# Kernel tuning notes

Hardware: AMD Instinct MI355X
Metric: run time of the kernel (lower is better)

The kernel has to match this reference:

```python
import jax, jax.numpy as jnp
import numpy as np

# Winograd F(2x2, 3x3) transform matrices (G matches the module's self.G)
_BT = np.array([[1, 0, -1, 0], [0, 1, 1, 0], [0, -1, 1, 0], [0, 1, 0, -1]], dtype=np.float32)
_G = np.array([[1, 0, 0], [0.5, 0.5, 0.5], [0.5, -0.5, 0.5], [0, 0, 1]], dtype=np.float32)
_AT = np.array([[1, 1, 1, 0], [0, 1, -1, -1]], dtype=np.float32)

PAD = 1  # module padding


def setup_inputs() -> dict:
    key = jax.random.key(0)
    k1, k2, k3 = jax.random.split(key, 3)
    x = jax.random.normal(k1, (16, 128, 112, 112), dtype=jnp.float32)
    weight = jax.random.normal(k2, (128, 128, 3, 3), dtype=jnp.float32) * 0.05
    bias = jax.random.normal(k3, (128,), dtype=jnp.float32) * 0.05
    return {"x": x, "weight": weight, "bias": bias}


def reference(x, weight, bias):
    # Winograd F(2x2,3x3) convolution, stride=1, padding=PAD.
    N, C, H, W = x.shape
    O = weight.shape[0]
    oh = H + 2 * PAD - 2
    ow = W + 2 * PAD - 2
    nth = -(-oh // 2)  # number of 2x2 output tiles along H
    ntw = -(-ow // 2)
    Hp = 2 * nth + 2  # padded size so every tile has a full 4x4 input patch
    Wp = 2 * ntw + 2
    xp = jnp.pad(x, ((0, 0), (0, 0), (PAD, Hp - H - PAD), (PAD, Wp - W - PAD)))

    # Gather overlapping 4x4 input tiles with stride 2 -> (N, C, nth, ntw, 4, 4)
    ih = (jnp.arange(nth) * 2)[:, None] + jnp.arange(4)[None, :]
    iw = (jnp.arange(ntw) * 2)[:, None] + jnp.arange(4)[None, :]
    tiles = xp[:, :, ih[:, None, :, None], iw[None, :, None, :]]

    Bt = jnp.asarray(_BT)
    G = jnp.asarray(_G)
    At = jnp.asarray(_AT)

    # Input transform: V = B^T d B   -> (N, C, nth, ntw, 4, 4)
    V = jnp.einsum('ij,nctujk,lk->nctuil', Bt, tiles, Bt)
    # Filter transform: U = G g G^T  -> (O, C, 4, 4)
    U = jnp.einsum('ij,ocjk,lk->ocil', G, weight, G)
    # Elementwise multiply in Winograd domain, contract over input channels
    M = jnp.einsum('ocij,nctuij->notuij', U, V)
    # Output transform: y = A^T M A  -> (N, O, nth, ntw, 2, 2)
    Yt = jnp.einsum('ai,notuij,bj->notuab', At, M, At)

    # Reassemble tiles into the output image and crop to (oh, ow)
    Y = Yt.transpose(0, 1, 2, 4, 3, 5).reshape(N, O, 2 * nth, 2 * ntw)[:, :, :oh, :ow]
    return Y + bias[None, :, None, None]
```

## Files before the change

kernel.cpp:

```cpp
#include <hip/hip_runtime.h>
#include <hip/hip_bf16.h>

typedef __bf16 bf16x8 __attribute__((ext_vector_type(8)));
typedef float f32x4 __attribute__((ext_vector_type(4)));

#define HH 112
#define WW 112
#define CIN 128
#define COUT 128

#define RR 18
#define RC 18
#define CSTRIDE 40

__global__ void wino_prep_weights(const float* __restrict__ w,
                                  __hip_bfloat16* __restrict__ wb) {
    int t = blockIdx.x * 256 + threadIdx.x;
    if (t >= 9 * COUT * CIN) return;
    int c = t & (CIN - 1);
    int o = (t >> 7) & (COUT - 1);
    int r = t >> 14;
    wb[t] = __float2bfloat16(w[(o * CIN + c) * 9 + r]);
}

__global__ __launch_bounds__(256, 2) void conv3x3_mfma(
        const float* __restrict__ x, const __hip_bfloat16* __restrict__ wb,
        const float* __restrict__ bias, float* __restrict__ out) {
    __shared__ __align__(16) __hip_bfloat16 xs[RR * RC * CSTRIDE];

    const int bx = blockIdx.x, by = blockIdx.y, n = blockIdx.z;
    const int ox0 = bx * 16, oy0 = by * 16;
    const int tid = threadIdx.x;
    const int lane = tid & 63;
    const int wv = tid >> 6;
    const int wo = wv >> 1;
    const int wp = wv & 1;
    const int l15 = lane & 15;
    const int lg = lane >> 4;

    f32x4 acc[4][8];
#pragma unroll
    for (int i = 0; i < 4; ++i)
#pragma unroll
        for (int j = 0; j < 8; ++j)
            acc[i][j] = (f32x4){0.f, 0.f, 0.f, 0.f};

#pragma unroll 1
    for (int cc = 0; cc < 4; ++cc) {
        if (cc) __syncthreads();
        const int cbase = cc * 32;
#pragma unroll
        for (int it = 0; it < 3; ++it) {
            int q = tid + it * 256;
            if (q < RR * 32) {
                int c = q & 31, row = q >> 5;
                int h = oy0 - 1 + row;
                const bool hok = (unsigned)h < (unsigned)HH;
                const float* src = x + (((size_t)(n * CIN + cbase + c) * HH + h) * WW) + (ox0 - 1);
                __hip_bfloat16* dst = xs + (row * RC) * CSTRIDE + c;
#pragma unroll
                for (int col = 0; col < RC; ++col) {
                    int wc = ox0 - 1 + col;
                    float v = 0.f;
                    if (hok && (unsigned)wc < (unsigned)WW) v = src[col];
                    dst[col * CSTRIDE] = __float2bfloat16(v);
                }
            }
        }
        __syncthreads();

#pragma unroll 1
        for (int off = 0; off < 9; ++off) {
            const int dy = (off * 11) >> 5;
            const int dx = off - dy * 3;
            bf16x8 af[4];
            const __hip_bfloat16* wbase =
                wb + ((size_t)(off * COUT) + wo * 64 + l15) * CIN + cbase + lg * 8;
#pragma unroll
            for (int os = 0; os < 4; ++os)
                af[os] = *reinterpret_cast<const bf16x8*>(wbase + os * 16 * CIN);
            bf16x8 bfr[8];
#pragma unroll
            for (int ps = 0; ps < 8; ++ps) {
                int cell = (wp * 8 + ps + dy) * RC + (l15 + dx);
                bfr[ps] = *reinterpret_cast<const bf16x8*>(xs + cell * CSTRIDE + lg * 8);
            }
#pragma unroll
            for (int os = 0; os < 4; ++os)
#pragma unroll
                for (int ps = 0; ps < 8; ++ps)
                    acc[os][ps] = __builtin_amdgcn_mfma_f32_16x16x32_bf16(
                        af[os], bfr[ps], acc[os][ps], 0, 0, 0);
        }
    }

#pragma unroll
    for (int os = 0; os < 4; ++os) {
#pragma unroll
        for (int r = 0; r < 4; ++r) {
            int o = wo * 64 + os * 16 + lg * 4 + r;
            float bv = bias[o];
            float* obase = out + (((size_t)(n * COUT + o) * HH + oy0) * WW) + ox0 + l15;
#pragma unroll
            for (int ps = 0; ps < 8; ++ps) {
                int py = wp * 8 + ps;
                obase[py * WW] = acc[os][ps][r] + bv;
            }
        }
    }
}

extern "C" void kernel_launch(void* const* d_in, const int* in_sizes, int n_in,
                              void* d_out, int out_size, void* d_ws, size_t ws_size,
                              hipStream_t stream) {
    const float* x = (const float*)d_in[0];
    const float* w = (const float*)d_in[1];
    const float* bias = (const float*)d_in[2];
    float* out = (float*)d_out;
    __hip_bfloat16* wb = (__hip_bfloat16*)d_ws;

    hipLaunchKernelGGL(wino_prep_weights, dim3(576), dim3(256), 0, stream, w, wb);
    hipLaunchKernelGGL(conv3x3_mfma, dim3(7, 7, 16), dim3(256), 0, stream,
                       x, wb, bias, out);
}
```

Baseline: 366.1 us.

## Pre-transpose input to padded NHWC bf16 and double-buffer async LDS loads

Adds a pre-pass that converts the NCHW fp32 input into a zero-padded NHWC bf16 buffer in workspace. The conv kernel then fills a double-buffered LDS tile with direct global-to-LDS 16-byte loads, overlapping the next channel chunk's load with the current chunk's MFMAs. This replaces the old per-element strided fp32 loads, conversions and bounds checks. Output tiles shrink to 8 rows, which doubles the grid and raises the occupancy hint to 3, at the cost of two extra kernel launches and a full extra pass over the input.

```diff
diff --git a/kernel.cpp b/kernel.cpp
--- a/kernel.cpp
+++ b/kernel.cpp
@@ -8,10 +8,11 @@
 #define WW 112
 #define CIN 128
 #define COUT 128
+#define HP 114
+#define WP 114
 
-#define RR 18
-#define RC 18
-#define CSTRIDE 40
+#define RRV 10
+#define RCV 18
 
 __global__ void wino_prep_weights(const float* __restrict__ w,
                                   __hip_bfloat16* __restrict__ wb) {
@@ -23,13 +24,52 @@
     wb[t] = __float2bfloat16(w[(o * CIN + c) * 9 + r]);
 }
 
-__global__ __launch_bounds__(256, 2) void conv3x3_mfma(
-        const float* __restrict__ x, const __hip_bfloat16* __restrict__ wb,
+__global__ void pad_borders(__hip_bfloat16* __restrict__ xt) {
+    int q = blockIdx.x * 256 + threadIdx.x;
+    int n = blockIdx.y;
+    if (q >= 452 * 16) return;
+    int chunk = q & 15;
+    int cell = q >> 4;
+    int hp, wp;
+    if (cell < 114)      { hp = 0;          wp = cell; }
+    else if (cell < 228) { hp = 113;        wp = cell - 114; }
+    else if (cell < 340) { hp = cell - 227; wp = 0; }
+    else                 { hp = cell - 339; wp = 113; }
+    bf16x8 z = {};
+    *reinterpret_cast<bf16x8*>(xt + ((size_t)(n * HP + hp) * WP + wp) * CIN + chunk * 8) = z;
+}
+
+__global__ __launch_bounds__(256) void transpose_pad(
+        const float* __restrict__ x, __hip_bfloat16* __restrict__ xt) {
+    const int wl = threadIdx.x & 15;
+    const int cg = threadIdx.x >> 4;
+    const int w = blockIdx.x * 16 + wl;
+    const int h = blockIdx.y;
+    const int n = blockIdx.z;
+    const float* src = x + (((size_t)(n * CIN + cg * 8) * HH + h) * WW) + w;
+    float v[8];
+#pragma unroll
+    for (int j = 0; j < 8; ++j) v[j] = src[(size_t)j * HH * WW];
+    union { bf16x8 v8; __hip_bfloat16 e[8]; } o;
+#pragma unroll
+    for (int j = 0; j < 8; ++j) o.e[j] = __float2bfloat16(v[j]);
+    *reinterpret_cast<bf16x8*>(
+        xt + ((size_t)(n * HP + h + 1) * WP + (w + 1)) * CIN + cg * 8) = o.v8;
+}
+
+__device__ __forceinline__ void gload_lds16(const __hip_bfloat16* g, __hip_bfloat16* l) {
+    __builtin_amdgcn_global_load_lds(
+        (const __attribute__((address_space(1))) unsigned int*)g,
+        (__attribute__((address_space(3))) unsigned int*)l, 16, 0, 0);
+}
+
+__global__ __launch_bounds__(256, 3) void conv3x3_mfma(
+        const __hip_bfloat16* __restrict__ xt, const __hip_bfloat16* __restrict__ wb,
         const float* __restrict__ bias, float* __restrict__ out) {
-    __shared__ __align__(16) __hip_bfloat16 xs[RR * RC * CSTRIDE];
+    __shared__ __align__(16) __hip_bfloat16 xs[2][RRV * RCV * 32];
 
-    const int bx = blockIdx.x, by = blockIdx.y, n = blockIdx.z;
-    const int ox0 = bx * 16, oy0 = by * 16;
+    const int ox0 = blockIdx.x * 16, oy0 = blockIdx.y * 8;
+    const int n = blockIdx.z;
     const int tid = threadIdx.x;
     const int lane = tid & 63;
     const int wv = tid >> 6;
@@ -38,38 +78,46 @@
     const int l15 = lane & 15;
     const int lg = lane >> 4;
 
-    f32x4 acc[4][8];
+    f32x4 acc[4][4];
 #pragma unroll
     for (int i = 0; i < 4; ++i)
 #pragma unroll
-        for (int j = 0; j < 8; ++j)
-            acc[i][j] = (f32x4){0.f, 0.f, 0.f, 0.f};
+        for (int j = 0; j < 4; ++j) acc[i][j] = (f32x4){0.f, 0.f, 0.f, 0.f};
+
+    const __hip_bfloat16* gb0 = xt + (((size_t)n * HP + oy0) * WP + ox0) * CIN;
+
+    int s_row[3], s_col[3], s_sub[3], s_act[3];
+#pragma unroll
+    for (int it = 0; it < 3; ++it) {
+        int q = tid + it * 256;
+        s_act[it] = (q < RRV * RCV * 4);
+        int cell = q >> 2;
+        int row = cell / RCV;
+        s_row[it] = row;
+        s_col[it] = cell - row * RCV;
+        s_sub[it] = q & 3;
+    }
+
+    auto stage = [&](int buf, int cc) {
+        const __hip_bfloat16* gb = gb0 + cc * 32;
+#pragma unroll
+        for (int it = 0; it < 3; ++it) {
+            int q = tid + it * 256;
+            if (s_act[it])
+                gload_lds16(gb + ((size_t)(s_row[it] * WP + s_col[it])) * CIN + s_sub[it] * 8,
+                            &xs[buf][q * 8]);
+        }
+    };
+
+    stage(0, 0);
+    __syncthreads();
 
 #pragma unroll 1
     for (int cc = 0; cc < 4; ++cc) {
-        if (cc) __syncthreads();
+        if (cc < 3) stage((cc + 1) & 1, cc + 1);
+        const int buf = cc & 1;
         const int cbase = cc * 32;
 #pragma unroll
-        for (int it = 0; it < 3; ++it) {
-            int q = tid + it * 256;
-            if (q < RR * 32) {
-                int c = q & 31, row = q >> 5;
-                int h = oy0 - 1 + row;
-                const bool hok = (unsigned)h < (unsigned)HH;
-                const float* src = x + (((size_t)(n * CIN + cbase + c) * HH + h) * WW) + (ox0 - 1);
-                __hip_bfloat16* dst = xs + (row * RC) * CSTRIDE + c;
-#pragma unroll
-                for (int col = 0; col < RC; ++col) {
-                    int wc = ox0 - 1 + col;
-                    float v = 0.f;
-                    if (hok && (unsigned)wc < (unsigned)WW) v = src[col];
-                    dst[col * CSTRIDE] = __float2bfloat16(v);
-                }
-            }
-        }
-        __syncthreads();
-
-#pragma unroll 1
         for (int off = 0; off < 9; ++off) {
             const int dy = (off * 11) >> 5;
             const int dx = off - dy * 3;
@@ -79,19 +127,22 @@
 #pragma unroll
             for (int os = 0; os < 4; ++os)
                 af[os] = *reinterpret_cast<const bf16x8*>(wbase + os * 16 * CIN);
-            bf16x8 bfr[8];
+            bf16x8 bfr[4];
 #pragma unroll
-            for (int ps = 0; ps < 8; ++ps) {
-                int cell = (wp * 8 + ps + dy) * RC + (l15 + dx);
-                bfr[ps] = *reinterpret_cast<const bf16x8*>(xs + cell * CSTRIDE + lg * 8);
+            for (int ps = 0; ps < 4; ++ps) {
+                int row = wp * 4 + ps + dy;
+                int col = l15 + dx;
+                bfr[ps] = *reinterpret_cast<const bf16x8*>(
+                    &xs[buf][((row * RCV + col) * 32) + lg * 8]);
             }
 #pragma unroll
             for (int os = 0; os < 4; ++os)
 #pragma unroll
-                for (int ps = 0; ps < 8; ++ps)
+                for (int ps = 0; ps < 4; ++ps)
                     acc[os][ps] = __builtin_amdgcn_mfma_f32_16x16x32_bf16(
                         af[os], bfr[ps], acc[os][ps], 0, 0, 0);
         }
+        __syncthreads();
     }
 
 #pragma unroll
@@ -100,12 +151,10 @@
         for (int r = 0; r < 4; ++r) {
             int o = wo * 64 + os * 16 + lg * 4 + r;
             float bv = bias[o];
-            float* obase = out + (((size_t)(n * COUT + o) * HH + oy0) * WW) + ox0 + l15;
+            float* obase = out + (((size_t)(n * COUT + o) * HH + oy0 + wp * 4) * WW) + ox0 + l15;
 #pragma unroll
-            for (int ps = 0; ps < 8; ++ps) {
-                int py = wp * 8 + ps;
-                obase[py * WW] = acc[os][ps][r] + bv;
-            }
+            for (int ps = 0; ps < 4; ++ps)
+                obase[ps * WW] = acc[os][ps][r] + bv;
         }
     }
 }
@@ -117,9 +166,13 @@
     const float* w = (const float*)d_in[1];
     const float* bias = (const float*)d_in[2];
     float* out = (float*)d_out;
-    __hip_bfloat16* wb = (__hip_bfloat16*)d_ws;
+
+    __hip_bfloat16* xt = (__hip_bfloat16*)d_ws;
+    __hip_bfloat16* wb = (__hip_bfloat16*)((char*)d_ws + 53231616);
 
     hipLaunchKernelGGL(wino_prep_weights, dim3(576), dim3(256), 0, stream, w, wb);
-    hipLaunchKernelGGL(conv3x3_mfma, dim3(7, 7, 16), dim3(256), 0, stream,
-                       x, wb, bias, out);
+    hipLaunchKernelGGL(pad_borders, dim3((452 * 16 + 255) / 256, 16), dim3(256), 0, stream, xt);
+    hipLaunchKernelGGL(transpose_pad, dim3(7, 112, 16), dim3(256), 0, stream, x, xt);
+    hipLaunchKernelGGL(conv3x3_mfma, dim3(7, 14, 16), dim3(256), 0, stream,
+                       xt, wb, bias, out);
 }
```

Result: faster. 335.6 us (-8.3%).
